# Optimization experiments

Hardware: AMD Instinct MI355X
Metric: run time of the kernel (lower is better)

## Reference

```python
import jax, jax.numpy as jnp
import numpy as np

B, S, E, H = 16, 512, 1024, 16
DK = E // H  # 64


def setup_inputs() -> dict:
    key = jax.random.key(0)
    ks = jax.random.split(key, 14)
    s_e = 1.0 / np.sqrt(E)
    s_d = 1.0 / np.sqrt(DK)
    return {
        "inp": jax.random.normal(ks[0], (B, S, E), dtype=jnp.float32),
        # projection linears (torch Linear stored as x @ W + b with W pre-transposed)
        "Wq": jax.random.uniform(ks[1], (E, E), jnp.float32, -s_e, s_e),
        "bq": jax.random.uniform(ks[2], (E,), jnp.float32, -s_e, s_e),
        "Wk": jax.random.uniform(ks[3], (E, E), jnp.float32, -s_e, s_e),
        "bk": jax.random.uniform(ks[4], (E,), jnp.float32, -s_e, s_e),
        "Wv": jax.random.uniform(ks[5], (E, E), jnp.float32, -s_e, s_e),
        "bv": jax.random.uniform(ks[6], (E,), jnp.float32, -s_e, s_e),
        # per-head gating linears
        "Wfq": jax.random.uniform(ks[7], (DK, DK), jnp.float32, -s_d, s_d),
        "bfq": jax.random.uniform(ks[8], (DK,), jnp.float32, -s_d, s_d),
        "Wfk": jax.random.uniform(ks[9], (DK, DK), jnp.float32, -s_d, s_d),
        "bfk": jax.random.uniform(ks[10], (DK,), jnp.float32, -s_d, s_d),
        "Wfg": jax.random.uniform(ks[11], (DK, 2 * DK), jnp.float32, -s_d, s_d),
        "bfg": jax.random.uniform(ks[12], (2 * DK,), jnp.float32, -s_d, s_d),
    }


def _split_heads(x):
    # [B, S, E] -> [B, H, S, DK]
    b, s, _ = x.shape
    return x.reshape(b, s, H, DK).transpose(0, 2, 1, 3)


def reference(inp, Wq, bq, Wk, bk, Wv, bv, Wfq, bfq, Wfk, bfk, Wfg, bfg):
    q = _split_heads(inp @ Wq + bq)  # [B,H,S,DK]
    k = _split_heads(inp @ Wk + bk)
    v = _split_heads(inp @ Wv + bv)

    # gated query/key modulation
    G = (q @ Wfq + bfq) * (k @ Wfk + bfk)          # [B,H,S,DK]
    M = jax.nn.sigmoid(G @ Wfg + bfg)              # [B,H,S,2*DK]
    q = q * M[..., :DK]
    k = k * M[..., DK:]

    scores = jnp.einsum("bhqd,bhkd->bhqk", q, k) / jnp.sqrt(jnp.asarray(DK, q.dtype))
    p_attn = jax.nn.softmax(scores, axis=-1)
    x = jnp.einsum("bhqk,bhkd->bhqd", p_attn, v)   # [B,H,S,DK]
    return x.transpose(0, 2, 1, 3).reshape(inp.shape[0], -1, H * DK)
```

## Files before the change

kernel.cpp:

```cpp
#include <hip/hip_runtime.h>


typedef __bf16 bf16;
typedef __bf16 bf16x8 __attribute__((ext_vector_type(8)));
typedef __bf16 bf16x4 __attribute__((ext_vector_type(4)));
typedef float  f32x4  __attribute__((ext_vector_type(4)));

#define MFMA16(a,b,c) __builtin_amdgcn_mfma_f32_16x16x32_bf16((a),(b),(c),0,0,0)

#define GLL16(gp, lp)                                                          \
  __builtin_amdgcn_global_load_lds(                                            \
      (__attribute__((address_space(1))) void*)(void*)(gp),                    \
      (__attribute__((address_space(3))) void*)(lp), 16, 0, 0)

__global__ __launch_bounds__(256) void k_prep(const float* __restrict__ in,
                                              bf16* __restrict__ Xb,
                                              const float* __restrict__ Wq,
                                              const float* __restrict__ Wk,
                                              const float* __restrict__ Wv,
                                              bf16* __restrict__ WT) {
  __shared__ float tile[32][33];
  const int bx = blockIdx.x, t = threadIdx.x;
  if (bx < 8192) {
    int i = bx * 256 + t;
    float4 v = ((const float4*)in)[i];
    bf16x4 o;
    o[0] = (bf16)v.x; o[1] = (bf16)v.y; o[2] = (bf16)v.z; o[3] = (bf16)v.w;
    ((bf16x4*)Xb)[i] = o;
  } else {
    int r = bx - 8192;
    int mat = r >> 10; r &= 1023;
    int kb = r >> 5, nb = r & 31;
    const float* W = (mat == 0) ? Wq : ((mat == 1) ? Wk : Wv);
    bf16* O = WT + (size_t)mat * (1024 * 1024);
    const int tr = t >> 3, tc = (t & 7) * 4;
    float4 v = *(const float4*)&W[(size_t)(kb * 32 + tr) * 1024 + nb * 32 + tc];
    tile[tr][tc] = v.x; tile[tr][tc + 1] = v.y;
    tile[tr][tc + 2] = v.z; tile[tr][tc + 3] = v.w;
    __syncthreads();
    bf16x4 o;
    o[0] = (bf16)tile[tc][tr];     o[1] = (bf16)tile[tc + 1][tr];
    o[2] = (bf16)tile[tc + 2][tr]; o[3] = (bf16)tile[tc + 3][tr];
    *(bf16x4*)&O[(size_t)(nb * 32 + tr) * 1024 + kb * 32 + tc] = o;
  }
}

__global__ __launch_bounds__(256, 2) void k_proj(const bf16* __restrict__ X,
                                                 const bf16* __restrict__ WT,
                                                 const float* __restrict__ bq,
                                                 const float* __restrict__ bk,
                                                 const float* __restrict__ bv,
                                                 bf16* __restrict__ qw,
                                                 bf16* __restrict__ kw,
                                                 bf16* __restrict__ vt) {
  extern __shared__ bf16 lds[];
  bf16* As = lds;
  bf16* Bs = lds + 16384;

  const int tid = threadIdx.x;
  const int m0 = blockIdx.x * 128;
  const int n0 = blockIdx.y * 192;

  const int l = tid & 63, wid = tid >> 6;
  const int wm = wid >> 1, wn = wid & 1;
  const int l4 = l & 15, q8 = l >> 4;
  const int cs0 = (q8 ^ (l4 & 7)) * 8;
  const int arow = (wm * 64 + l4) * 64;
  const int brow = (wn * 96 + l4) * 64;

  const int srow = tid >> 3;
  const int scol = ((tid & 7) ^ (srow & 7)) * 8;
  const bf16* Xs = X + (size_t)(m0 + srow) * 1024 + scol;
  const bf16* Ws = WT + (size_t)(n0 + srow) * 1024 + scol;
  const int ldst = tid * 8;

#define STG_AU(bf, kt, u)                                                      \
  GLL16(Xs + (size_t)(u) * 32768 + (kt) * 64,                                  \
        As + (bf) * 8192 + (u) * 2048 + ldst)
#define STG_BU(bf, kt, u)                                                      \
  GLL16(Ws + (size_t)(u) * 32768 + (kt) * 64,                                  \
        Bs + (bf) * 12288 + (u) * 2048 + ldst)

  f32x4 acc[4][6] = {};
  bf16x8 aa[2], bb0[6], bb1[6];

#define LDA2(bf, qm, kk)                                                       \
  do {                                                                         \
    _Pragma("unroll") for (int m_ = 0; m_ < 2; ++m_)                           \
        aa[m_] = *(const bf16x8*)&As[(bf) * 8192 + arow + (qm) * 2048 +        \
                                     m_ * 1024 + (cs0 ^ ((kk) * 32))];         \
  } while (0)
#define LDB6(bf, kk, arr)                                                      \
  do {                                                                         \
    _Pragma("unroll") for (int n_ = 0; n_ < 6; ++n_)                           \
        arr[n_] = *(const bf16x8*)&Bs[(bf) * 12288 + brow + n_ * 1024 +        \
                                      (cs0 ^ ((kk) * 32))];                    \
  } while (0)
#define MMQ(qm, arr)                                                           \
  do {                                                                         \
    _Pragma("unroll") for (int m_ = 0; m_ < 2; ++m_)                           \
    _Pragma("unroll") for (int n_ = 0; n_ < 6; ++n_)                           \
        acc[(qm) * 2 + m_][n_] =                                               \
            MFMA16(arr[n_], aa[m_], acc[(qm) * 2 + m_][n_]);                   \
  } while (0)
#define PH_PRE                                                                 \
  __builtin_amdgcn_s_barrier();                                                \
  asm volatile("s_waitcnt lgkmcnt(0)" ::: "memory");                           \
  __builtin_amdgcn_s_setprio(1)
#define PH_POST                                                                \
  __builtin_amdgcn_s_setprio(0);                                               \
  __builtin_amdgcn_s_barrier()

  STG_AU(0, 0, 0); STG_AU(0, 0, 1); STG_AU(0, 0, 2); STG_AU(0, 0, 3);
  STG_BU(0, 0, 0); STG_BU(0, 0, 1); STG_BU(0, 0, 2);
  STG_BU(0, 0, 3); STG_BU(0, 0, 4); STG_BU(0, 0, 5);
  STG_BU(1, 1, 0); STG_BU(1, 1, 1); STG_BU(1, 1, 2);
  STG_BU(1, 1, 3); STG_BU(1, 1, 4); STG_BU(1, 1, 5);
  asm volatile("s_waitcnt vmcnt(6)" ::: "memory");
  __builtin_amdgcn_s_barrier();

#pragma unroll 1
  for (int i = 0; i < 8; ++i) {
    const int t1 = 2 * i + 1;
    const int t2 = (i < 7) ? 2 * i + 2 : 14;
    const int t3 = (i < 7) ? 2 * i + 3 : 15;
    LDB6(0, 0, bb0); LDA2(0, 0, 0);
    STG_AU(1, t1, 0); STG_AU(1, t1, 1);
    PH_PRE; MMQ(0, bb0); PH_POST;
    LDB6(0, 1, bb1); LDA2(0, 1, 0);
    STG_AU(1, t1, 2); STG_AU(1, t1, 3);
    PH_PRE; MMQ(1, bb0); PH_POST;
    LDA2(0, 0, 1);
    STG_BU(0, t2, 0); STG_BU(0, t2, 1); STG_BU(0, t2, 2);
    PH_PRE; MMQ(0, bb1); PH_POST;
    LDA2(0, 1, 1);
    STG_BU(0, t2, 3); STG_BU(0, t2, 4); STG_BU(0, t2, 5);
    PH_PRE; MMQ(1, bb1);
    __builtin_amdgcn_s_setprio(0);
    asm volatile("s_waitcnt vmcnt(6)" ::: "memory");
    __builtin_amdgcn_s_barrier();
    LDB6(1, 0, bb0); LDA2(1, 0, 0);
    STG_AU(0, t2, 0); STG_AU(0, t2, 1);
    PH_PRE; MMQ(0, bb0); PH_POST;
    LDB6(1, 1, bb1); LDA2(1, 1, 0);
    STG_AU(0, t2, 2); STG_AU(0, t2, 3);
    PH_PRE; MMQ(1, bb0); PH_POST;
    LDA2(1, 0, 1);
    STG_BU(1, t3, 0); STG_BU(1, t3, 1); STG_BU(1, t3, 2);
    PH_PRE; MMQ(0, bb1); PH_POST;
    LDA2(1, 1, 1);
    STG_BU(1, t3, 3); STG_BU(1, t3, 4); STG_BU(1, t3, 5);
    PH_PRE; MMQ(1, bb1);
    __builtin_amdgcn_s_setprio(0);
    asm volatile("s_waitcnt vmcnt(6)" ::: "memory");
    __builtin_amdgcn_s_barrier();
  }

#pragma unroll
  for (int mi = 0; mi < 4; ++mi) {
    const int m = m0 + wm * 64 + mi * 16 + l4;
    const int b_ = m >> 9, s = m & 511;
#pragma unroll
    for (int nj = 0; nj < 6; ++nj) {
      const int n = n0 + wn * 96 + nj * 16 + q8 * 4;
      const int mat = n >> 10, nn = n & 1023;
      if (mat == 2) {
        const int h = nn >> 6, d0 = nn & 63;
#pragma unroll
        for (int r = 0; r < 4; ++r) {
          vt[((size_t)(b_ * 16 + h) * 64 + d0 + r) * 512 + s] =
              (bf16)(acc[mi][nj][r] + bv[nn + r]);
        }
      } else {
        const float* bias = (mat == 0) ? bq : bk;
        const float4 bb = *(const float4*)&bias[nn];
        bf16x4 o;
        o[0] = (bf16)(acc[mi][nj][0] + bb.x);
        o[1] = (bf16)(acc[mi][nj][1] + bb.y);
        o[2] = (bf16)(acc[mi][nj][2] + bb.z);
        o[3] = (bf16)(acc[mi][nj][3] + bb.w);
        bf16* dst = (mat == 0) ? qw : kw;
        *(bf16x4*)&dst[(size_t)m * 1024 + nn] = o;
      }
    }
  }
#undef STG_AU
#undef STG_BU
#undef LDA2
#undef LDB6
#undef MMQ
#undef PH_PRE
#undef PH_POST
}

__global__ __launch_bounds__(256, 2) void k_gate(bf16* __restrict__ qw,
                                                 bf16* __restrict__ kw,
                                                 const float* __restrict__ Wfq,
                                                 const float* __restrict__ bfq,
                                                 const float* __restrict__ Wfk,
                                                 const float* __restrict__ bfk,
                                                 const float* __restrict__ Wfg,
                                                 const float* __restrict__ bfg) {
  __shared__ __align__(16) char smraw[56320];
  bf16* sWq = (bf16*)smraw;
  bf16* sWk = (bf16*)(smraw + 9216);
  bf16* sWg = (bf16*)(smraw + 18432);
  bf16* sG  = (bf16*)(smraw + 36864);
  float* sb = (float*)(smraw + 55296);
  bf16* Ms  = (bf16*)smraw;
  const int tid = threadIdx.x;

  for (int idx = tid; idx < 4096; idx += 256) {
    int k = idx >> 6, n = idx & 63;
    sWq[n * 72 + k] = (bf16)Wfq[k * 64 + n];
    sWk[n * 72 + k] = (bf16)Wfk[k * 64 + n];
  }
  for (int idx = tid; idx < 8192; idx += 256) {
    int k = idx >> 7, n = idx & 127;
    sWg[n * 72 + k] = (bf16)Wfg[k * 128 + n];
  }
  if (tid < 64) { sb[tid] = bfq[tid]; sb[64 + tid] = bfk[tid]; }
  if (tid < 128) sb[128 + tid] = bfg[tid];
  __syncthreads();

  const int w = tid >> 6, l = tid & 63, l4 = l & 15, q8 = l >> 4;
  const int T0 = blockIdx.x * 128;
  const int rbase = w * 32;

  bf16x8 aq[2][2], ak[2][2];
#pragma unroll
  for (int i = 0; i < 2; ++i)
#pragma unroll
    for (int kk = 0; kk < 2; ++kk) {
      size_t off = (size_t)(T0 + rbase + i * 16 + l4) * 64 + kk * 32 + q8 * 8;
      aq[i][kk] = *(const bf16x8*)&qw[off];
      ak[i][kk] = *(const bf16x8*)&kw[off];
    }

  f32x4 fqc[2][4] = {}, fkc[2][4] = {};
#pragma unroll
  for (int j = 0; j < 4; ++j) {
    bf16x8 bq0 = *(const bf16x8*)&sWq[(j * 16 + l4) * 72 + q8 * 8];
    bf16x8 bq1 = *(const bf16x8*)&sWq[(j * 16 + l4) * 72 + 32 + q8 * 8];
    bf16x8 bk0 = *(const bf16x8*)&sWk[(j * 16 + l4) * 72 + q8 * 8];
    bf16x8 bk1 = *(const bf16x8*)&sWk[(j * 16 + l4) * 72 + 32 + q8 * 8];
#pragma unroll
    for (int i = 0; i < 2; ++i) {
      fqc[i][j] = MFMA16(aq[i][0], bq0, fqc[i][j]);
      fqc[i][j] = MFMA16(aq[i][1], bq1, fqc[i][j]);
      fkc[i][j] = MFMA16(ak[i][0], bk0, fkc[i][j]);
      fkc[i][j] = MFMA16(ak[i][1], bk1, fkc[i][j]);
    }
  }

#pragma unroll
  for (int j = 0; j < 4; ++j) {
    float bqb = sb[j * 16 + l4], bkb = sb[64 + j * 16 + l4];
#pragma unroll
    for (int i = 0; i < 2; ++i)
#pragma unroll
      for (int r = 0; r < 4; ++r) {
        int row = rbase + i * 16 + q8 * 4 + r;
        float g = (fqc[i][j][r] + bqb) * (fkc[i][j][r] + bkb);
        sG[row * 72 + j * 16 + l4] = (bf16)g;
      }
  }
  __syncthreads();

  bf16x8 ag[2][2];
#pragma unroll
  for (int i = 0; i < 2; ++i)
#pragma unroll
    for (int kk = 0; kk < 2; ++kk)
      ag[i][kk] = *(const bf16x8*)&sG[(rbase + i * 16 + l4) * 72 + kk * 32 + q8 * 8];
  f32x4 mc[2][8] = {};
#pragma unroll
  for (int jj = 0; jj < 8; ++jj) {
    bf16x8 bg0 = *(const bf16x8*)&sWg[(jj * 16 + l4) * 72 + q8 * 8];
    bf16x8 bg1 = *(const bf16x8*)&sWg[(jj * 16 + l4) * 72 + 32 + q8 * 8];
#pragma unroll
    for (int i = 0; i < 2; ++i) {
      mc[i][jj] = MFMA16(ag[i][0], bg0, mc[i][jj]);
      mc[i][jj] = MFMA16(ag[i][1], bg1, mc[i][jj]);
    }
  }

  __syncthreads();
#pragma unroll
  for (int jj = 0; jj < 8; ++jj) {
    float bgb = sb[128 + jj * 16 + l4];
#pragma unroll
    for (int i = 0; i < 2; ++i)
#pragma unroll
      for (int r = 0; r < 4; ++r) {
        int row = rbase + i * 16 + q8 * 4 + r;
        float m = mc[i][jj][r] + bgb;
        Ms[row * 136 + jj * 16 + l4] = (bf16)(1.0f / (1.0f + __expf(-m)));
      }
  }
  __syncthreads();

  const float SC = 0.18033688011112042f;
  const int tl = tid >> 1, half = tid & 1;
  bf16* base = (half ? kw : qw) + (size_t)(T0 + tl) * 64;
  const float scl = half ? 1.0f : SC;
#pragma unroll
  for (int c = 0; c < 8; ++c) {
    bf16x8 v = *(const bf16x8*)&base[c * 8];
    bf16x8 m = *(const bf16x8*)&Ms[tl * 136 + half * 64 + c * 8];
    bf16x8 o;
#pragma unroll
    for (int e = 0; e < 8; ++e)
      o[e] = (bf16)((float)v[e] * (float)m[e] * scl);
    *(bf16x8*)&base[c * 8] = o;
  }
}

__global__ __launch_bounds__(256, 2) void k_attn(const bf16* __restrict__ qw,
                                                 const bf16* __restrict__ kw,
                                                 const bf16* __restrict__ vt,
                                                 float* __restrict__ out) {
  __shared__ bf16 Kt[128 * 72];
  __shared__ bf16 Vt[64 * 136];
  const int tid = threadIdx.x, w = tid >> 6, l = tid & 63;
  const int l4 = l & 15, q8 = l >> 4;
  const int bx = blockIdx.x;
  const int slot = bx >> 3;
  const int qc = slot & 3;
  const int bh = (bx & 7) + 8 * (slot >> 2);
  const int b_ = bh >> 4, h = bh & 15;
  bf16* Pw = Kt + w * 1280;

  bf16x8 qf[2][2];
#pragma unroll
  for (int i = 0; i < 2; ++i)
#pragma unroll
    for (int kk = 0; kk < 2; ++kk) {
      int s = qc * 128 + w * 32 + i * 16 + l4;
      qf[i][kk] = *(const bf16x8*)
          &qw[(((size_t)b_ * 512 + s) * 16 + h) * 64 + kk * 32 + q8 * 8];
    }

  f32x4 o[2][4] = {};
  float mrun[2][4], lrun[2][4];
#pragma unroll
  for (int i = 0; i < 2; ++i)
#pragma unroll
    for (int r = 0; r < 4; ++r) { mrun[i][r] = -3.0e38f; lrun[i][r] = 0.0f; }

  for (int t = 0; t < 4; ++t) {
    __syncthreads();
#pragma unroll
    for (int i = 0; i < 4; ++i) {
      int chunk = i * 256 + tid;
      {
        int key = chunk >> 3, c8 = chunk & 7;
        bf16x8 v = *(const bf16x8*)
            &kw[(((size_t)b_ * 512 + t * 128 + key) * 16 + h) * 64 + c8 * 8];
        *(bf16x8*)&Kt[key * 72 + c8 * 8] = v;
      }
      {
        int d = chunk >> 4, c16 = chunk & 15;
        bf16x8 v = *(const bf16x8*)
            &vt[((size_t)bh * 64 + d) * 512 + t * 128 + c16 * 8];
        *(bf16x8*)&Vt[d * 136 + c16 * 8] = v;
      }
    }
    __syncthreads();

    f32x4 sc[2][8];
    const f32x4 fz = {};
    __builtin_amdgcn_s_setprio(1);
#pragma unroll
    for (int c = 0; c < 8; ++c) {
      bf16x8 kb0 = *(const bf16x8*)&Kt[(c * 16 + l4) * 72 + q8 * 8];
      sc[0][c] = MFMA16(qf[0][0], kb0, fz);
      sc[1][c] = MFMA16(qf[1][0], kb0, fz);
      bf16x8 kb1 = *(const bf16x8*)&Kt[(c * 16 + l4) * 72 + 32 + q8 * 8];
      sc[0][c] = MFMA16(qf[0][1], kb1, sc[0][c]);
      sc[1][c] = MFMA16(qf[1][1], kb1, sc[1][c]);
    }
    __builtin_amdgcn_s_setprio(0);
    __syncthreads();

#pragma unroll
    for (int i = 0; i < 2; ++i) {
      float mx[4];
#pragma unroll
      for (int r = 0; r < 4; ++r) {
        float m2 = sc[i][0][r];
#pragma unroll
        for (int c = 1; c < 8; ++c) m2 = fmaxf(m2, sc[i][c][r]);
        m2 = fmaxf(m2, __shfl_xor(m2, 1));
        m2 = fmaxf(m2, __shfl_xor(m2, 2));
        m2 = fmaxf(m2, __shfl_xor(m2, 4));
        m2 = fmaxf(m2, __shfl_xor(m2, 8));
        mx[r] = m2;
      }
      bool grow = false;
#pragma unroll
      for (int r = 0; r < 4; ++r) grow = grow || (mx[r] > mrun[i][r] + 8.0f);
      if (__any(grow)) {
        float al[4];
#pragma unroll
        for (int r = 0; r < 4; ++r) {
          float mn = fmaxf(mrun[i][r], mx[r]);
          al[r] = exp2f(mrun[i][r] - mn);
          mrun[i][r] = mn;
          lrun[i][r] *= al[r];
        }
#pragma unroll
        for (int f = 0; f < 4; ++f)
#pragma unroll
          for (int r = 0; r < 4; ++r) o[i][f][r] *= al[r];
      }
#pragma unroll
      for (int r = 0; r < 4; ++r) {
        float sm = 0.0f;
#pragma unroll
        for (int c = 0; c < 8; ++c) {
          float p = exp2f(sc[i][c][r] - mrun[i][r]);
          sc[i][c][r] = p;
          sm += p;
        }
        sm += __shfl_xor(sm, 1); sm += __shfl_xor(sm, 2);
        sm += __shfl_xor(sm, 4); sm += __shfl_xor(sm, 8);
        lrun[i][r] += sm;
      }
    }

#pragma unroll
    for (int kk2 = 0; kk2 < 4; ++kk2) {
#pragma unroll
      for (int i = 0; i < 2; ++i)
#pragma unroll
        for (int cc = 0; cc < 2; ++cc) {
          int c = kk2 * 2 + cc;
#pragma unroll
          for (int r = 0; r < 4; ++r)
            Pw[(i * 16 + q8 * 4 + r) * 40 + cc * 16 + l4] = (bf16)sc[i][c][r];
        }
      bf16x8 pa0 = *(const bf16x8*)&Pw[(l4) * 40 + q8 * 8];
      bf16x8 pa1 = *(const bf16x8*)&Pw[(16 + l4) * 40 + q8 * 8];
      __builtin_amdgcn_s_setprio(1);
#pragma unroll
      for (int f = 0; f < 4; ++f) {
        bf16x8 vb = *(const bf16x8*)&Vt[(f * 16 + l4) * 136 + kk2 * 32 + q8 * 8];
        o[0][f] = MFMA16(pa0, vb, o[0][f]);
        o[1][f] = MFMA16(pa1, vb, o[1][f]);
      }
      __builtin_amdgcn_s_setprio(0);
    }
  }

#pragma unroll
  for (int i = 0; i < 2; ++i)
#pragma unroll
    for (int r = 0; r < 4; ++r) {
      int srow = qc * 128 + w * 32 + i * 16 + q8 * 4 + r;
      float inv = 1.0f / lrun[i][r];
#pragma unroll
      for (int f = 0; f < 4; ++f)
        out[(((size_t)b_ * 512 + srow) * 16 + h) * 64 + f * 16 + l4] =
            o[i][f][r] * inv;
    }
}

extern "C" void kernel_launch(void* const* d_in, const int* in_sizes, int n_in,
                              void* d_out, int out_size, void* d_ws,
                              size_t ws_size, hipStream_t stream) {
  (void)in_sizes; (void)n_in; (void)out_size; (void)ws_size;
  const float* inp = (const float*)d_in[0];
  const float* Wq  = (const float*)d_in[1];
  const float* bq  = (const float*)d_in[2];
  const float* Wk  = (const float*)d_in[3];
  const float* bk  = (const float*)d_in[4];
  const float* Wv  = (const float*)d_in[5];
  const float* bv  = (const float*)d_in[6];
  const float* Wfq = (const float*)d_in[7];
  const float* bfq = (const float*)d_in[8];
  const float* Wfk = (const float*)d_in[9];
  const float* bfk = (const float*)d_in[10];
  const float* Wfg = (const float*)d_in[11];
  const float* bfg = (const float*)d_in[12];
  float* out = (float*)d_out;

  static bool s_attr = false;
  if (!s_attr) {
    (void)hipFuncSetAttribute((const void*)k_proj,
                              hipFuncAttributeMaxDynamicSharedMemorySize,
                              81920);
    s_attr = true;
  }

  char* ws = (char*)d_ws;
  bf16* Xb = (bf16*)(ws);
  bf16* WT = (bf16*)(ws + 16777216);
  bf16* qw = (bf16*)(ws + 16777216 + 6291456);
  bf16* kw = qw + 8388608;
  bf16* vt = kw + 8388608;

  k_prep<<<11264, 256, 0, stream>>>(inp, Xb, Wq, Wk, Wv, WT);
  k_proj<<<dim3(64, 16), 256, 81920, stream>>>(Xb, WT, bq, bk, bv, qw, kw, vt);
  k_gate<<<1024, 256, 0, stream>>>(qw, kw, Wfq, bfq, Wfk, bfk, Wfg, bfg);
  k_attn<<<1024, 256, 0, stream>>>(qw, kw, vt, out);
}
```

Measured before the change: 249.8 us.

## Fuse gating into projection GEMM by remapping N-tiles to per-head QKV

Each projection block's 192 output columns now correspond to one head's Q, K and V slices rather than a contiguous column range. That lets the epilogue stage Q and K in LDS, run the gate linears, the sigmoid and the modulation in place, and write the final gated q/k directly. This removes the separate k_gate launch and its global read-modify-write of q and k. The cost is a longer GEMM epilogue with extra barriers and per-block reloading of the small gate weights into LDS.

```diff
diff --git a/kernel.cpp b/kernel.cpp
--- a/kernel.cpp
+++ b/kernel.cpp
@@ -50,6 +50,12 @@
                                                  const float* __restrict__ bq,
                                                  const float* __restrict__ bk,
                                                  const float* __restrict__ bv,
+                                                 const float* __restrict__ Wfq,
+                                                 const float* __restrict__ bfq,
+                                                 const float* __restrict__ Wfk,
+                                                 const float* __restrict__ bfk,
+                                                 const float* __restrict__ Wfg,
+                                                 const float* __restrict__ bfg,
                                                  bf16* __restrict__ qw,
                                                  bf16* __restrict__ kw,
                                                  bf16* __restrict__ vt) {
@@ -59,7 +65,7 @@
 
   const int tid = threadIdx.x;
   const int m0 = blockIdx.x * 128;
-  const int n0 = blockIdx.y * 192;
+  const int h  = blockIdx.y;
 
   const int l = tid & 63, wid = tid >> 6;
   const int wm = wid >> 1, wn = wid & 1;
@@ -70,15 +76,18 @@
 
   const int srow = tid >> 3;
   const int scol = ((tid & 7) ^ (srow & 7)) * 8;
-  const bf16* Xs = X + (size_t)(m0 + srow) * 1024 + scol;
-  const bf16* Ws = WT + (size_t)(n0 + srow) * 1024 + scol;
+  const bf16* Xs  = X  + (size_t)(m0 + srow) * 1024 + scol;
+  const bf16* Wq_ = WT + (size_t)(h * 64 + srow) * 1024 + scol;
+  const bf16* Wk_ = Wq_ + (size_t)1024 * 1024;
+  const bf16* Wv_ = Wk_ + (size_t)1024 * 1024;
   const int ldst = tid * 8;
 
 #define STG_AU(bf, kt, u)                                                      \
   GLL16(Xs + (size_t)(u) * 32768 + (kt) * 64,                                  \
         As + (bf) * 8192 + (u) * 2048 + ldst)
+#define BSRC(u) ((u) < 2 ? Wq_ : ((u) < 4 ? Wk_ : Wv_))
 #define STG_BU(bf, kt, u)                                                      \
-  GLL16(Ws + (size_t)(u) * 32768 + (kt) * 64,                                  \
+  GLL16(BSRC(u) + (size_t)((u) & 1) * 32768 + (kt) * 64,                       \
         Bs + (bf) * 12288 + (u) * 2048 + ldst)
 
   f32x4 acc[4][6] = {};
@@ -156,164 +165,162 @@
     __builtin_amdgcn_s_barrier();
   }
 
+  asm volatile("s_waitcnt vmcnt(0)" ::: "memory");
+  __syncthreads();
+
+  char* gb = (char*)lds;
+  bf16* sQ  = (bf16*)gb;
+  bf16* sK  = (bf16*)(gb + 18432);
+  bf16* sWq = (bf16*)(gb + 36864);
+  bf16* sWk = (bf16*)(gb + 46080);
+  bf16* sWg = (bf16*)(gb + 55296);
+  float* sb = (float*)(gb + 73728);
+  bf16* sG  = (bf16*)(gb + 36864);
+  bf16* Ms  = (bf16*)(gb + 36864);
+
+  for (int idx = tid; idx < 4096; idx += 256) {
+    int k = idx >> 6, n = idx & 63;
+    sWq[n * 72 + k] = (bf16)Wfq[k * 64 + n];
+    sWk[n * 72 + k] = (bf16)Wfk[k * 64 + n];
+  }
+  for (int idx = tid; idx < 8192; idx += 256) {
+    int k = idx >> 7, n = idx & 127;
+    sWg[n * 72 + k] = (bf16)Wfg[k * 128 + n];
+  }
+  if (tid < 64) { sb[tid] = bfq[tid]; sb[64 + tid] = bfk[tid]; }
+  if (tid < 128) sb[128 + tid] = bfg[tid];
+
 #pragma unroll
   for (int mi = 0; mi < 4; ++mi) {
-    const int m = m0 + wm * 64 + mi * 16 + l4;
+    const int tok = wm * 64 + mi * 16 + l4;
+    const int m = m0 + tok;
     const int b_ = m >> 9, s = m & 511;
 #pragma unroll
     for (int nj = 0; nj < 6; ++nj) {
-      const int n = n0 + wn * 96 + nj * 16 + q8 * 4;
-      const int mat = n >> 10, nn = n & 1023;
-      if (mat == 2) {
-        const int h = nn >> 6, d0 = nn & 63;
-#pragma unroll
-        for (int r = 0; r < 4; ++r) {
-          vt[((size_t)(b_ * 16 + h) * 64 + d0 + r) * 512 + s] =
-              (bf16)(acc[mi][nj][r] + bv[nn + r]);
-        }
+      if (wn == 1 && nj >= 2) {
+        const int dv = (nj - 2) * 16 + q8 * 4;
+        const float4 bb = *(const float4*)&bv[h * 64 + dv];
+#pragma unroll
+        for (int r = 0; r < 4; ++r)
+          vt[((size_t)(b_ * 16 + h) * 64 + dv + r) * 512 + s] =
+              (bf16)(acc[mi][nj][r] + ((const float*)&bb)[r]);
       } else {
-        const float* bias = (mat == 0) ? bq : bk;
-        const float4 bb = *(const float4*)&bias[nn];
+        const bool isq = (wn == 0 && nj < 4);
+        const int d = isq ? (nj * 16 + q8 * 4)
+                          : (wn == 0 ? (nj - 4) * 16 + q8 * 4
+                                     : 32 + nj * 16 + q8 * 4);
+        const float* bsrc = isq ? bq : bk;
+        const float4 bb = *(const float4*)&bsrc[h * 64 + d];
         bf16x4 o;
         o[0] = (bf16)(acc[mi][nj][0] + bb.x);
         o[1] = (bf16)(acc[mi][nj][1] + bb.y);
         o[2] = (bf16)(acc[mi][nj][2] + bb.z);
         o[3] = (bf16)(acc[mi][nj][3] + bb.w);
-        bf16* dst = (mat == 0) ? qw : kw;
-        *(bf16x4*)&dst[(size_t)m * 1024 + nn] = o;
-      }
-    }
+        *(bf16x4*)&((isq ? sQ : sK)[tok * 72 + d]) = o;
+      }
+    }
+  }
+  __syncthreads();
+
+  const int rbase = wid * 32;
+  bf16x8 aq[2][2], ak[2][2];
+#pragma unroll
+  for (int i = 0; i < 2; ++i)
+#pragma unroll
+    for (int kk = 0; kk < 2; ++kk) {
+      const int off = (rbase + i * 16 + l4) * 72 + kk * 32 + q8 * 8;
+      aq[i][kk] = *(const bf16x8*)&sQ[off];
+      ak[i][kk] = *(const bf16x8*)&sK[off];
+    }
+  f32x4 fqc[2][4] = {}, fkc[2][4] = {};
+#pragma unroll
+  for (int j = 0; j < 4; ++j) {
+    bf16x8 bq0 = *(const bf16x8*)&sWq[(j * 16 + l4) * 72 + q8 * 8];
+    bf16x8 bq1 = *(const bf16x8*)&sWq[(j * 16 + l4) * 72 + 32 + q8 * 8];
+    bf16x8 bk0 = *(const bf16x8*)&sWk[(j * 16 + l4) * 72 + q8 * 8];
+    bf16x8 bk1 = *(const bf16x8*)&sWk[(j * 16 + l4) * 72 + 32 + q8 * 8];
+#pragma unroll
+    for (int i = 0; i < 2; ++i) {
+      fqc[i][j] = MFMA16(aq[i][0], bq0, fqc[i][j]);
+      fqc[i][j] = MFMA16(aq[i][1], bq1, fqc[i][j]);
+      fkc[i][j] = MFMA16(ak[i][0], bk0, fkc[i][j]);
+      fkc[i][j] = MFMA16(ak[i][1], bk1, fkc[i][j]);
+    }
+  }
+  __syncthreads();
+
+#pragma unroll
+  for (int j = 0; j < 4; ++j) {
+    float bqb = sb[j * 16 + l4], bkb = sb[64 + j * 16 + l4];
+#pragma unroll
+    for (int i = 0; i < 2; ++i)
+#pragma unroll
+      for (int r = 0; r < 4; ++r) {
+        int row = rbase + i * 16 + q8 * 4 + r;
+        float g = (fqc[i][j][r] + bqb) * (fkc[i][j][r] + bkb);
+        sG[row * 72 + j * 16 + l4] = (bf16)g;
+      }
+  }
+  __syncthreads();
+
+  bf16x8 ag[2][2];
+#pragma unroll
+  for (int i = 0; i < 2; ++i)
+#pragma unroll
+    for (int kk = 0; kk < 2; ++kk)
+      ag[i][kk] = *(const bf16x8*)&sG[(rbase + i * 16 + l4) * 72 + kk * 32 + q8 * 8];
+  f32x4 mc[2][8] = {};
+#pragma unroll
+  for (int jj = 0; jj < 8; ++jj) {
+    bf16x8 bg0 = *(const bf16x8*)&sWg[(jj * 16 + l4) * 72 + q8 * 8];
+    bf16x8 bg1 = *(const bf16x8*)&sWg[(jj * 16 + l4) * 72 + 32 + q8 * 8];
+#pragma unroll
+    for (int i = 0; i < 2; ++i) {
+      mc[i][jj] = MFMA16(ag[i][0], bg0, mc[i][jj]);
+      mc[i][jj] = MFMA16(ag[i][1], bg1, mc[i][jj]);
+    }
+  }
+  __syncthreads();
+
+#pragma unroll
+  for (int jj = 0; jj < 8; ++jj) {
+    float bgb = sb[128 + jj * 16 + l4];
+#pragma unroll
+    for (int i = 0; i < 2; ++i)
+#pragma unroll
+      for (int r = 0; r < 4; ++r) {
+        int row = rbase + i * 16 + q8 * 4 + r;
+        float m = mc[i][jj][r] + bgb;
+        Ms[row * 136 + jj * 16 + l4] = (bf16)(1.0f / (1.0f + __expf(-m)));
+      }
+  }
+  __syncthreads();
+
+  const float SCg = 0.18033688011112042f;
+  const int tl = tid >> 1, half = tid & 1;
+  const int mg = m0 + tl;
+  bf16* dstg = (half ? kw : qw) + (size_t)mg * 1024 + h * 64;
+  const bf16* srcg = (half ? sK : sQ) + tl * 72;
+  const bf16* msg_ = Ms + tl * 136 + half * 64;
+  const float scl = half ? 1.0f : SCg;
+#pragma unroll
+  for (int c = 0; c < 8; ++c) {
+    bf16x8 v = *(const bf16x8*)&srcg[c * 8];
+    bf16x8 m = *(const bf16x8*)&msg_[c * 8];
+    bf16x8 o;
+#pragma unroll
+    for (int e = 0; e < 8; ++e)
+      o[e] = (bf16)((float)v[e] * (float)m[e] * scl);
+    *(bf16x8*)&dstg[c * 8] = o;
   }
 #undef STG_AU
 #undef STG_BU
+#undef BSRC
 #undef LDA2
 #undef LDB6
 #undef MMQ
 #undef PH_PRE
 #undef PH_POST
-}
-
-__global__ __launch_bounds__(256, 2) void k_gate(bf16* __restrict__ qw,
-                                                 bf16* __restrict__ kw,
-                                                 const float* __restrict__ Wfq,
-                                                 const float* __restrict__ bfq,
-                                                 const float* __restrict__ Wfk,
-                                                 const float* __restrict__ bfk,
-                                                 const float* __restrict__ Wfg,
-                                                 const float* __restrict__ bfg) {
-  __shared__ __align__(16) char smraw[56320];
-  bf16* sWq = (bf16*)smraw;
-  bf16* sWk = (bf16*)(smraw + 9216);
-  bf16* sWg = (bf16*)(smraw + 18432);
-  bf16* sG  = (bf16*)(smraw + 36864);
-  float* sb = (float*)(smraw + 55296);
-  bf16* Ms  = (bf16*)smraw;
-  const int tid = threadIdx.x;
-
-  for (int idx = tid; idx < 4096; idx += 256) {
-    int k = idx >> 6, n = idx & 63;
-    sWq[n * 72 + k] = (bf16)Wfq[k * 64 + n];
-    sWk[n * 72 + k] = (bf16)Wfk[k * 64 + n];
-  }
-  for (int idx = tid; idx < 8192; idx += 256) {
-    int k = idx >> 7, n = idx & 127;
-    sWg[n * 72 + k] = (bf16)Wfg[k * 128 + n];
-  }
-  if (tid < 64) { sb[tid] = bfq[tid]; sb[64 + tid] = bfk[tid]; }
-  if (tid < 128) sb[128 + tid] = bfg[tid];
-  __syncthreads();
-
-  const int w = tid >> 6, l = tid & 63, l4 = l & 15, q8 = l >> 4;
-  const int T0 = blockIdx.x * 128;
-  const int rbase = w * 32;
-
-  bf16x8 aq[2][2], ak[2][2];
-#pragma unroll
-  for (int i = 0; i < 2; ++i)
-#pragma unroll
-    for (int kk = 0; kk < 2; ++kk) {
-      size_t off = (size_t)(T0 + rbase + i * 16 + l4) * 64 + kk * 32 + q8 * 8;
-      aq[i][kk] = *(const bf16x8*)&qw[off];
-      ak[i][kk] = *(const bf16x8*)&kw[off];
-    }
-
-  f32x4 fqc[2][4] = {}, fkc[2][4] = {};
-#pragma unroll
-  for (int j = 0; j < 4; ++j) {
-    bf16x8 bq0 = *(const bf16x8*)&sWq[(j * 16 + l4) * 72 + q8 * 8];
-    bf16x8 bq1 = *(const bf16x8*)&sWq[(j * 16 + l4) * 72 + 32 + q8 * 8];
-    bf16x8 bk0 = *(const bf16x8*)&sWk[(j * 16 + l4) * 72 + q8 * 8];
-    bf16x8 bk1 = *(const bf16x8*)&sWk[(j * 16 + l4) * 72 + 32 + q8 * 8];
-#pragma unroll
-    for (int i = 0; i < 2; ++i) {
-      fqc[i][j] = MFMA16(aq[i][0], bq0, fqc[i][j]);
-      fqc[i][j] = MFMA16(aq[i][1], bq1, fqc[i][j]);
-      fkc[i][j] = MFMA16(ak[i][0], bk0, fkc[i][j]);
-      fkc[i][j] = MFMA16(ak[i][1], bk1, fkc[i][j]);
-    }
-  }
-
-#pragma unroll
-  for (int j = 0; j < 4; ++j) {
-    float bqb = sb[j * 16 + l4], bkb = sb[64 + j * 16 + l4];
-#pragma unroll
-    for (int i = 0; i < 2; ++i)
-#pragma unroll
-      for (int r = 0; r < 4; ++r) {
-        int row = rbase + i * 16 + q8 * 4 + r;
-        float g = (fqc[i][j][r] + bqb) * (fkc[i][j][r] + bkb);
-        sG[row * 72 + j * 16 + l4] = (bf16)g;
-      }
-  }
-  __syncthreads();
-
-  bf16x8 ag[2][2];
-#pragma unroll
-  for (int i = 0; i < 2; ++i)
-#pragma unroll
-    for (int kk = 0; kk < 2; ++kk)
-      ag[i][kk] = *(const bf16x8*)&sG[(rbase + i * 16 + l4) * 72 + kk * 32 + q8 * 8];
-  f32x4 mc[2][8] = {};
-#pragma unroll
-  for (int jj = 0; jj < 8; ++jj) {
-    bf16x8 bg0 = *(const bf16x8*)&sWg[(jj * 16 + l4) * 72 + q8 * 8];
-    bf16x8 bg1 = *(const bf16x8*)&sWg[(jj * 16 + l4) * 72 + 32 + q8 * 8];
-#pragma unroll
-    for (int i = 0; i < 2; ++i) {
-      mc[i][jj] = MFMA16(ag[i][0], bg0, mc[i][jj]);
-      mc[i][jj] = MFMA16(ag[i][1], bg1, mc[i][jj]);
-    }
-  }
-
-  __syncthreads();
-#pragma unroll
-  for (int jj = 0; jj < 8; ++jj) {
-    float bgb = sb[128 + jj * 16 + l4];
-#pragma unroll
-    for (int i = 0; i < 2; ++i)
-#pragma unroll
-      for (int r = 0; r < 4; ++r) {
-        int row = rbase + i * 16 + q8 * 4 + r;
-        float m = mc[i][jj][r] + bgb;
-        Ms[row * 136 + jj * 16 + l4] = (bf16)(1.0f / (1.0f + __expf(-m)));
-      }
-  }
-  __syncthreads();
-
-  const float SC = 0.18033688011112042f;
-  const int tl = tid >> 1, half = tid & 1;
-  bf16* base = (half ? kw : qw) + (size_t)(T0 + tl) * 64;
-  const float scl = half ? 1.0f : SC;
-#pragma unroll
-  for (int c = 0; c < 8; ++c) {
-    bf16x8 v = *(const bf16x8*)&base[c * 8];
-    bf16x8 m = *(const bf16x8*)&Ms[tl * 136 + half * 64 + c * 8];
-    bf16x8 o;
-#pragma unroll
-    for (int e = 0; e < 8; ++e)
-      o[e] = (bf16)((float)v[e] * (float)m[e] * scl);
-    *(bf16x8*)&base[c * 8] = o;
-  }
 }
 
 __global__ __launch_bounds__(256, 2) void k_attn(const bf16* __restrict__ qw,
@@ -501,7 +508,8 @@
   bf16* vt = kw + 8388608;
 
   k_prep<<<11264, 256, 0, stream>>>(inp, Xb, Wq, Wk, Wv, WT);
-  k_proj<<<dim3(64, 16), 256, 81920, stream>>>(Xb, WT, bq, bk, bv, qw, kw, vt);
-  k_gate<<<1024, 256, 0, stream>>>(qw, kw, Wfq, bfq, Wfk, bfk, Wfg, bfg);
+  k_proj<<<dim3(64, 16), 256, 81920, stream>>>(Xb, WT, bq, bk, bv,
+                                               Wfq, bfq, Wfk, bfk, Wfg, bfg,
+                                               qw, kw, vt);
   k_attn<<<1024, 256, 0, stream>>>(qw, kw, vt, out);
 }
```

New measurement: 228.8 us. 1.09x faster.
